# Performance work log

Measured on AMD Instinct MI355X. Metric: run time of the kernel, lower is better.

## Reference

```python
import jax, jax.numpy as jnp
import numpy as np
import math

B, S, H, NH, DH, FF, L = 2, 1024, 768, 12, 64, 3072, 4
LN_EPS = 1e-12


def _layer_norm(x, g, b):
    m = jnp.mean(x, axis=-1, keepdims=True)
    v = jnp.mean(jnp.square(x - m), axis=-1, keepdims=True)
    return (x - m) * jax.lax.rsqrt(v + LN_EPS) * g + b


def _gelu(x):
    # BERT erf-based gelu: x * 0.5 * (1 + erf(x / sqrt(2)))
    return x * 0.5 * (1.0 + jax.lax.erf(x / jnp.sqrt(jnp.asarray(2.0, x.dtype))))


def setup_inputs() -> dict:
    key = jax.random.key(0)
    ks = jax.random.split(key, 10)
    init = lambda k, shape: (jax.random.normal(k, shape, jnp.float32) * 0.02)
    inp = {
        'x': jax.random.normal(ks[0], (B, S, H), jnp.float32),
        'mask': jax.random.randint(ks[1], (B, S, S), 0, 2).astype(jnp.int32),
        'Wq': init(ks[2], (L, H, H)), 'bq': jnp.zeros((L, H), jnp.float32),
        'Wk': init(ks[3], (L, H, H)), 'bk': jnp.zeros((L, H), jnp.float32),
        'Wv': init(ks[4], (L, H, H)), 'bv': jnp.zeros((L, H), jnp.float32),
        'Wao': init(ks[5], (L, H, H)), 'bao': jnp.zeros((L, H), jnp.float32),
        'g1': jnp.ones((L, H), jnp.float32), 'b1': jnp.zeros((L, H), jnp.float32),
        'Wi': init(ks[6], (L, H, FF)), 'bi': jnp.zeros((L, FF), jnp.float32),
        'Wfo': init(ks[7], (L, FF, H)), 'bfo': jnp.zeros((L, H), jnp.float32),
        'g2': jnp.ones((L, H), jnp.float32), 'b2': jnp.zeros((L, H), jnp.float32),
    }
    return inp


def reference(x, mask, Wq, bq, Wk, bk, Wv, bv, Wao, bao, g1, b1, Wi, bi, Wfo, bfo, g2, b2):
    # additive mask: (1 - mask) * -10000, broadcast over heads -> [B,1,S,S]
    adder = (1.0 - mask.astype(x.dtype))[:, None, :, :] * -10000.0
    scale = 1.0 / math.sqrt(DH)

    def block(h, p):
        (wq, bq_, wk, bk_, wv, bv_, wao, bao_, g1_, b1_, wi, bi_, wfo, bfo_, g2_, b2_) = p
        q = (h @ wq + bq_).reshape(B, S, NH, DH)
        k = (h @ wk + bk_).reshape(B, S, NH, DH)
        v = (h @ wv + bv_).reshape(B, S, NH, DH)
        scores = jnp.einsum('bqhd,bkhd->bhqk', q, k) * scale + adder
        probs = jax.nn.softmax(scores, axis=-1)
        ctx = jnp.einsum('bhqk,bkhd->bqhd', probs, v).reshape(B, S, H)
        attn_out = _layer_norm(ctx @ wao + bao_ + h, g1_, b1_)
        inter = _gelu(attn_out @ wi + bi_)
        out = _layer_norm(inter @ wfo + bfo_ + attn_out, g2_, b2_)
        return out, None

    params = (Wq, bq, Wk, bk, Wv, bv, Wao, bao, g1, b1, Wi, bi, Wfo, bfo, g2, b2)
    out, _ = jax.lax.scan(block, x, params)
    return out
```

## Files before the change

kernel.cpp:

```cpp
#include <hip/hip_runtime.h>
#include <math.h>

#define B_  2
#define S_  1024
#define H_  768
#define NH_ 12
#define DH_ 64
#define FF_ 3072
#define L_  4

typedef short v8s __attribute__((ext_vector_type(8)));
typedef float v4f __attribute__((ext_vector_type(4)));

static __device__ __forceinline__ unsigned short f2bf(float f) {
    unsigned int u = __float_as_uint(f);
    unsigned int r = (u + 0x7fffu + ((u >> 16) & 1u)) >> 16;
    return (unsigned short)r;
}
static __device__ __forceinline__ float bf2f(unsigned short u) {
    return __uint_as_float((unsigned int)u << 16);
}

#define GLOAD16(g, l) __builtin_amdgcn_global_load_lds( \
    (const __attribute__((address_space(1))) unsigned int*)(g), \
    (__attribute__((address_space(3))) unsigned int*)(l), 16, 0, 0)

__global__ void conv_bf16_k(const float* __restrict__ in, unsigned short* __restrict__ out, int n) {
    int i = blockIdx.x * 256 + threadIdx.x;
    if (i < n) out[i] = f2bf(in[i]);
}

__global__ void maskconv_k(const int* __restrict__ m, unsigned short* __restrict__ o, int n) {
    int i = blockIdx.x * 256 + threadIdx.x;
    if (i < n) o[i] = m[i] ? (unsigned short)0u : (unsigned short)0xC661u;
}

__global__ __launch_bounds__(256) void transpose_convert(
    const float* __restrict__ W, unsigned short* __restrict__ Wt,
    int K, int N, size_t in_lstride, size_t out_lstride)
{
    __shared__ float tile[32][33];
    const int l = blockIdx.z;
    const float* src = W + (size_t)l * in_lstride;
    unsigned short* dst = Wt + (size_t)l * out_lstride;
    const int k0 = blockIdx.x * 32;
    const int n0 = blockIdx.y * 32;
    const int t = threadIdx.x;
    const int tc = t & 31, tr = t >> 5;
#pragma unroll
    for (int i = 0; i < 4; ++i) {
        int r = tr + i * 8;
        tile[r][tc] = src[(size_t)(k0 + r) * N + n0 + tc];
    }
    __syncthreads();
#pragma unroll
    for (int i = 0; i < 4; ++i) {
        int r = tr + i * 8;
        dst[(size_t)(n0 + r) * K + k0 + tc] = f2bf(tile[tc][r]);
    }
}

template<int ACT, int OUT_BF, int NBIAS, int SPLIT>
__global__ __launch_bounds__(256) void gemm_k(
    const unsigned short* __restrict__ A,
    const unsigned short* __restrict__ Bt,
    const float* __restrict__ b0,
    const float* __restrict__ b1,
    const float* __restrict__ b2,
    const float* __restrict__ res,
    void* __restrict__ out0,
    float* __restrict__ out1,
    int M, int N, int K, int klen)
{
    __shared__ __align__(16) unsigned short As[2][128 * 64];
    __shared__ __align__(16) unsigned short Bs[2][64 * 64];
    const int t = threadIdx.x;
    const int m0 = blockIdx.x * 128;
    const int n0 = blockIdx.y * 64;
    const int kz = SPLIT ? blockIdx.z : 0;
    const int kstart = kz * klen;
    const int lane = t & 63;
    const int w = t >> 6;
    const int wm = w >> 1, wn = w & 1;
    const int l15 = lane & 15;
    const int q4  = lane >> 4;

    const unsigned short* gA[4];
    const unsigned short* gB[2];
#pragma unroll
    for (int i = 0; i < 4; ++i) {
        int c = t + i * 256;
        int r = c >> 3, cc = c & 7;
        gA[i] = A + (size_t)(m0 + r) * K + kstart + ((cc ^ (r & 7)) << 3);
    }
#pragma unroll
    for (int i = 0; i < 2; ++i) {
        int c = t + i * 256;
        int r = c >> 3, cc = c & 7;
        gB[i] = Bt + (size_t)(n0 + r) * K + kstart + ((cc ^ (r & 7)) << 3);
    }
    const int ldsW = w * 512;

    v4f acc[4][2] = {};
    const int nt = klen >> 6;

#pragma unroll
    for (int i = 0; i < 4; ++i) GLOAD16(gA[i], &As[0][i * 2048 + ldsW]);
#pragma unroll
    for (int i = 0; i < 2; ++i) GLOAD16(gB[i], &Bs[0][i * 2048 + ldsW]);

    int cur = 0;
    for (int kt = 0; kt < nt; ++kt) {
        __syncthreads();
        if (kt + 1 < nt) {
            const size_t go = (size_t)(kt + 1) << 6;
#pragma unroll
            for (int i = 0; i < 4; ++i) GLOAD16(gA[i] + go, &As[cur ^ 1][i * 2048 + ldsW]);
#pragma unroll
            for (int i = 0; i < 2; ++i) GLOAD16(gB[i] + go, &Bs[cur ^ 1][i * 2048 + ldsW]);
        }
        const unsigned short* as = As[cur];
        const unsigned short* bs = Bs[cur];
#pragma unroll
        for (int ks = 0; ks < 2; ++ks) {
            v8s af[4], bf[2];
#pragma unroll
            for (int i = 0; i < 4; ++i) {
                int r = wm * 64 + i * 16 + l15;
                af[i] = *(const v8s*)&as[r * 64 + ((((ks << 2) + q4) ^ (r & 7)) << 3)];
            }
#pragma unroll
            for (int i = 0; i < 2; ++i) {
                int r = wn * 32 + i * 16 + l15;
                bf[i] = *(const v8s*)&bs[r * 64 + ((((ks << 2) + q4) ^ (r & 7)) << 3)];
            }
#pragma unroll
            for (int fm = 0; fm < 4; ++fm)
#pragma unroll
                for (int fn = 0; fn < 2; ++fn)
                    acc[fm][fn] = __builtin_amdgcn_mfma_f32_16x16x32_bf16(af[fm], bf[fn], acc[fm][fn], 0, 0, 0);
        }
        cur ^= 1;
    }

    const int rb = q4 * 4;
#pragma unroll
    for (int fm = 0; fm < 4; ++fm)
#pragma unroll
        for (int fn = 0; fn < 2; ++fn)
#pragma unroll
            for (int i = 0; i < 4; ++i) {
                const int row = m0 + wm * 64 + fm * 16 + rb + i;
                const int col = n0 + wn * 32 + fn * 16 + l15;
                float v = acc[fm][fn][i];
                const size_t oi = (size_t)row * N + col;
                if (!SPLIT || kz == 0) {
                    float bb;
                    if (NBIAS == 3) {
                        int which = (col >= 1536) ? 2 : (col >= 768 ? 1 : 0);
                        const float* bp = (which == 0) ? b0 : ((which == 1) ? b1 : b2);
                        bb = bp[col - which * 768];
                    } else {
                        bb = b0[col];
                    }
                    v += bb;
                    if (res) v += res[oi];
                    if (ACT == 1) v = 0.5f * v * (1.0f + erff(v * 0.70710678118654752f));
                    if (OUT_BF) ((unsigned short*)out0)[oi] = f2bf(v);
                    else        ((float*)out0)[oi] = v;
                } else {
                    out1[oi] = v;
                }
            }
}

__global__ __launch_bounds__(256) void ln_k(
    const float* __restrict__ ina, const float* __restrict__ inb,
    const float* __restrict__ g, const float* __restrict__ be,
    float* __restrict__ outf, unsigned short* __restrict__ outb)
{
    const int row = blockIdx.x;
    const float* xa = ina + (size_t)row * H_;
    const float* xb = inb + (size_t)row * H_;
    const int t = threadIdx.x;
    const int wave = t >> 6, lane = t & 63;
    float v0 = xa[t] + xb[t];
    float v1 = xa[t + 256] + xb[t + 256];
    float v2 = xa[t + 512] + xb[t + 512];
    float s = v0 + v1 + v2;
    float s2 = v0 * v0 + v1 * v1 + v2 * v2;
#pragma unroll
    for (int o = 32; o; o >>= 1) { s += __shfl_xor(s, o); s2 += __shfl_xor(s2, o); }
    __shared__ float rs[4], rq[4];
    if (lane == 0) { rs[wave] = s; rq[wave] = s2; }
    __syncthreads();
    s  = rs[0] + rs[1] + rs[2] + rs[3];
    s2 = rq[0] + rq[1] + rq[2] + rq[3];
    const float mean = s * (1.0f / 768.0f);
    float var = s2 * (1.0f / 768.0f) - mean * mean;
    var = fmaxf(var, 0.0f);
    const float inv = rsqrtf(var + 1e-12f);
#pragma unroll
    for (int i = 0; i < 3; ++i) {
        int c = t + i * 256;
        float vv = (i == 0) ? v0 : ((i == 1) ? v1 : v2);
        float y = (vv - mean) * inv * g[c] + be[c];
        outf[(size_t)row * H_ + c] = y;
        outb[(size_t)row * H_ + c] = f2bf(y);
    }
}

__global__ __launch_bounds__(256) void fattn_k(
    const unsigned short* __restrict__ qkv,
    const unsigned short* __restrict__ madd,
    float* __restrict__ pO,
    float* __restrict__ pML)
{
    const int qt = blockIdx.x, h = blockIdx.y, zz = blockIdx.z;
    const int b = zz >> 1, kvh = zz & 1;
    const int q0 = qt * 64;
    const int t = threadIdx.x;
    const int w = t >> 6, lane = t & 63;
    const int l15 = lane & 15;
    const int kr8 = (lane >> 4) * 8;
    const int rb  = (lane >> 4) * 4;
    const int wq0 = w * 16;

    __shared__ __align__(16) unsigned short Ks[64][72];
    __shared__ __align__(16) unsigned short Vt[4096];
    __shared__ __align__(16) unsigned short Ps[64][72];

    const size_t rstr = 2304;
    const unsigned short* base = qkv + (size_t)b * S_ * rstr + h * 64;

    v8s qf0, qf1;
    {
        const unsigned short* qp = base + (size_t)(q0 + wq0 + l15) * rstr + kr8;
        qf0 = *(const v8s*)qp;
        qf1 = *(const v8s*)(qp + 32);
    }

    const int skp = t >> 3;
    const int sd0 = (t & 7) * 8;
    const unsigned short* kbase = base + 768  + (size_t)(kvh * 512 + skp) * rstr + sd0;
    const unsigned short* vbase = base + 1536 + (size_t)(kvh * 512 + 2 * skp) * rstr + sd0;
    const size_t kstep = (size_t)64 * rstr;

    float m_[4], l_[4];
    v4f accO[4];
#pragma unroll
    for (int i = 0; i < 4; ++i) { m_[i] = -3.0e38f; l_[i] = 0.f; }
#pragma unroll
    for (int f = 0; f < 4; ++f) accO[f] = (v4f){0.f, 0.f, 0.f, 0.f};

    const unsigned short* mrow[4];
#pragma unroll
    for (int i = 0; i < 4; ++i)
        mrow[i] = madd + ((size_t)(b * S_) + q0 + wq0 + rb + i) * S_ + kvh * 512;

    v8s kA0, kA1, vA0, vA1, kB0, kB1, vB0, vB1;
    kA0 = *(const v8s*)(kbase);
    kA1 = *(const v8s*)(kbase + 32 * rstr);
    vA0 = *(const v8s*)(vbase);
    vA1 = *(const v8s*)(vbase + rstr);

    const float SC2 = 0.18033688011112042f;

    for (int kt = 0; kt < 8; ++kt) {
        const int k0 = kt * 64;
        unsigned short mu[16];
#pragma unroll
        for (int f = 0; f < 4; ++f)
#pragma unroll
            for (int i = 0; i < 4; ++i)
                mu[f * 4 + i] = mrow[i][k0 + f * 16 + l15];

        __syncthreads();
        if ((kt & 1) == 0) {
            *(v8s*)&Ks[skp][sd0] = kA0;
            *(v8s*)&Ks[skp + 32][sd0] = kA1;
#pragma unroll
            for (int j = 0; j < 8; ++j) {
                const int d = sd0 + j;
                const int sw = ((d & 7) ^ (d >> 3)) << 3;
                unsigned int pk = ((unsigned int)(unsigned short)vA1[j] << 16) | (unsigned short)vA0[j];
                *(unsigned int*)&Vt[(size_t)d * 64 + ((2 * skp) ^ sw)] = pk;
            }
            if (kt < 7) {
                const unsigned short* kp = kbase + (size_t)(kt + 1) * kstep;
                const unsigned short* vp = vbase + (size_t)(kt + 1) * kstep;
                kB0 = *(const v8s*)kp;
                kB1 = *(const v8s*)(kp + 32 * rstr);
                vB0 = *(const v8s*)vp;
                vB1 = *(const v8s*)(vp + rstr);
            }
        } else {
            *(v8s*)&Ks[skp][sd0] = kB0;
            *(v8s*)&Ks[skp + 32][sd0] = kB1;
#pragma unroll
            for (int j = 0; j < 8; ++j) {
                const int d = sd0 + j;
                const int sw = ((d & 7) ^ (d >> 3)) << 3;
                unsigned int pk = ((unsigned int)(unsigned short)vB1[j] << 16) | (unsigned short)vB0[j];
                *(unsigned int*)&Vt[(size_t)d * 64 + ((2 * skp) ^ sw)] = pk;
            }
            if (kt < 7) {
                const unsigned short* kp = kbase + (size_t)(kt + 1) * kstep;
                const unsigned short* vp = vbase + (size_t)(kt + 1) * kstep;
                kA0 = *(const v8s*)kp;
                kA1 = *(const v8s*)(kp + 32 * rstr);
                vA0 = *(const v8s*)vp;
                vA1 = *(const v8s*)(vp + rstr);
            }
        }
        __syncthreads();

        v4f s4[4];
#pragma unroll
        for (int f = 0; f < 4; ++f) s4[f] = (v4f){0.f, 0.f, 0.f, 0.f};
#pragma unroll
        for (int ks = 0; ks < 2; ++ks) {
            v8s qv = ks ? qf1 : qf0;
#pragma unroll
            for (int f = 0; f < 4; ++f) {
                v8s kf = *(const v8s*)&Ks[f * 16 + l15][ks * 32 + kr8];
                s4[f] = __builtin_amdgcn_mfma_f32_16x16x32_bf16(qv, kf, s4[f], 0, 0, 0);
            }
        }

        float p[4][4];
        float mx[4];
#pragma unroll
        for (int i = 0; i < 4; ++i) mx[i] = -3.0e38f;
#pragma unroll
        for (int f = 0; f < 4; ++f)
#pragma unroll
            for (int i = 0; i < 4; ++i) {
                float v = s4[f][i] * SC2 + bf2f(mu[f * 4 + i]);
                p[f][i] = v;
                mx[i] = fmaxf(mx[i], v);
            }
#pragma unroll
        for (int o = 8; o; o >>= 1)
#pragma unroll
            for (int i = 0; i < 4; ++i) mx[i] = fmaxf(mx[i], __shfl_xor(mx[i], o));
        float corr[4], rsum[4];
#pragma unroll
        for (int i = 0; i < 4; ++i) {
            float mn = fmaxf(m_[i], mx[i]);
            corr[i] = exp2f(m_[i] - mn);
            m_[i] = mn;
            rsum[i] = 0.f;
        }
#pragma unroll
        for (int f = 0; f < 4; ++f)
#pragma unroll
            for (int i = 0; i < 4; ++i) {
                float e = exp2f(p[f][i] - m_[i]);
                p[f][i] = e;
                rsum[i] += e;
            }
#pragma unroll
        for (int o = 8; o; o >>= 1)
#pragma unroll
            for (int i = 0; i < 4; ++i) rsum[i] += __shfl_xor(rsum[i], o);
#pragma unroll
        for (int i = 0; i < 4; ++i) l_[i] = l_[i] * corr[i] + rsum[i];
#pragma unroll
        for (int f = 0; f < 4; ++f)
#pragma unroll
            for (int i = 0; i < 4; ++i) accO[f][i] *= corr[i];

#pragma unroll
        for (int f = 0; f < 4; ++f)
#pragma unroll
            for (int i = 0; i < 4; ++i)
                Ps[wq0 + rb + i][f * 16 + l15] = f2bf(p[f][i]);

#pragma unroll
        for (int ks = 0; ks < 2; ++ks) {
            v8s pf = *(const v8s*)&Ps[wq0 + l15][ks * 32 + kr8];
#pragma unroll
            for (int f = 0; f < 4; ++f) {
                const int d = f * 16 + l15;
                const int sw = ((d & 7) ^ (d >> 3)) << 3;
                v8s vf = *(const v8s*)&Vt[(size_t)d * 64 + ((ks * 32 + kr8) ^ sw)];
                accO[f] = __builtin_amdgcn_mfma_f32_16x16x32_bf16(pf, vf, accO[f], 0, 0, 0);
            }
        }
    }

    float* po = pO + (size_t)kvh * (2048 * 768);
#pragma unroll
    for (int f = 0; f < 4; ++f)
#pragma unroll
        for (int i = 0; i < 4; ++i) {
            size_t row = (size_t)(b * S_) + q0 + wq0 + rb + i;
            po[row * 768 + h * 64 + f * 16 + l15] = accO[f][i];
        }
    if (l15 == 0) {
#pragma unroll
        for (int i = 0; i < 4; ++i) {
            size_t row = (size_t)(b * S_) + q0 + wq0 + rb + i;
            size_t idx = (((size_t)kvh * 2048 + row) * NH_ + h) * 2;
            pML[idx] = m_[i];
            pML[idx + 1] = l_[i];
        }
    }
}

__global__ __launch_bounds__(256) void attn_merge(
    const float* __restrict__ pO, const float* __restrict__ pML,
    unsigned short* __restrict__ ctx)
{
    const int i = blockIdx.x * 256 + threadIdx.x;
    const int row = i / 192;
    const int c4 = (i - row * 192) * 4;
    const int h = c4 >> 6;
    const size_t mi0 = ((size_t)row * NH_ + h) * 2;
    const size_t mi1 = (((size_t)2048 + row) * NH_ + h) * 2;
    const float m0 = pML[mi0], l0 = pML[mi0 + 1];
    const float m1 = pML[mi1], l1 = pML[mi1 + 1];
    const float mm = fmaxf(m0, m1);
    const float c0 = exp2f(m0 - mm), c1 = exp2f(m1 - mm);
    const float inv = 1.0f / (l0 * c0 + l1 * c1);
    const size_t off = (size_t)row * 768 + c4;
    float4 o0 = *(const float4*)&pO[off];
    float4 o1 = *(const float4*)&pO[(size_t)2048 * 768 + off];
    unsigned short r[4];
    r[0] = f2bf((o0.x * c0 + o1.x * c1) * inv);
    r[1] = f2bf((o0.y * c0 + o1.y * c1) * inv);
    r[2] = f2bf((o0.z * c0 + o1.z * c1) * inv);
    r[3] = f2bf((o0.w * c0 + o1.w * c1) * inv);
    *(uint2*)&ctx[off] = *(uint2*)r;
}

extern "C" void kernel_launch(void* const* d_in, const int* in_sizes, int n_in,
                              void* d_out, int out_size, void* d_ws, size_t ws_size,
                              hipStream_t stream)
{
    const float* x   = (const float*)d_in[0];
    const int*   mask= (const int*)  d_in[1];
    const float* Wq  = (const float*)d_in[2];
    const float* bq  = (const float*)d_in[3];
    const float* Wk  = (const float*)d_in[4];
    const float* bk  = (const float*)d_in[5];
    const float* Wv  = (const float*)d_in[6];
    const float* bv  = (const float*)d_in[7];
    const float* Wao = (const float*)d_in[8];
    const float* bao = (const float*)d_in[9];
    const float* g1  = (const float*)d_in[10];
    const float* b1  = (const float*)d_in[11];
    const float* Wi  = (const float*)d_in[12];
    const float* bi  = (const float*)d_in[13];
    const float* Wfo = (const float*)d_in[14];
    const float* bfo = (const float*)d_in[15];
    const float* g2  = (const float*)d_in[16];
    const float* b2  = (const float*)d_in[17];
    float* out = (float*)d_out;

    const int M = B_ * S_;
    char* basep = (char*)d_ws;
    size_t off = 0;
    auto alloc = [&](size_t bytes) -> char* {
        char* p = basep + off;
        off = (off + bytes + 255) & ~(size_t)255;
        return p;
    };

    unsigned short* WqkvT = (unsigned short*)alloc((size_t)L_ * 2304 * 768 * 2);
    unsigned short* WaoT  = (unsigned short*)alloc((size_t)L_ * 768 * 768 * 2);
    unsigned short* WiT   = (unsigned short*)alloc((size_t)L_ * 3072 * 768 * 2);
    unsigned short* WfoT  = (unsigned short*)alloc((size_t)L_ * 768 * 3072 * 2);
    unsigned short* h_bf  = (unsigned short*)alloc((size_t)M * 768 * 2);
    unsigned short* qkvbf = (unsigned short*)alloc((size_t)M * 2304 * 2);
    unsigned short* ctxbf = (unsigned short*)alloc((size_t)M * 768 * 2);
    float* t1a            = (float*)alloc((size_t)M * 768 * 4);
    float* attnf          = (float*)alloc((size_t)M * 768 * 4);
    unsigned short* attnbf= (unsigned short*)alloc((size_t)M * 768 * 2);
    unsigned short* interbf = (unsigned short*)alloc((size_t)M * FF_ * 2);
    unsigned short* madd  = (unsigned short*)alloc((size_t)B_ * S_ * S_ * 2);
    float* t1b = (float*)(void*)qkvbf;
    float* pO  = (float*)(void*)interbf;
    float* pML = t1a;

    dim3 tb(256);
    transpose_convert<<<dim3(24, 24, L_), tb, 0, stream>>>(Wq,  WqkvT + 0,          768,  768, (size_t)768 * 768,  (size_t)2304 * 768);
    transpose_convert<<<dim3(24, 24, L_), tb, 0, stream>>>(Wk,  WqkvT + 768 * 768,  768,  768, (size_t)768 * 768,  (size_t)2304 * 768);
    transpose_convert<<<dim3(24, 24, L_), tb, 0, stream>>>(Wv,  WqkvT + 1536 * 768, 768,  768, (size_t)768 * 768,  (size_t)2304 * 768);
    transpose_convert<<<dim3(24, 24, L_), tb, 0, stream>>>(Wao, WaoT,               768,  768, (size_t)768 * 768,  (size_t)768 * 768);
    transpose_convert<<<dim3(24, 96, L_), tb, 0, stream>>>(Wi,  WiT,                768, 3072, (size_t)768 * 3072, (size_t)3072 * 768);
    transpose_convert<<<dim3(96, 24, L_), tb, 0, stream>>>(Wfo, WfoT,              3072,  768, (size_t)3072 * 768, (size_t)768 * 3072);

    conv_bf16_k<<<(M * 768 + 255) / 256, 256, 0, stream>>>(x, h_bf, M * 768);
    maskconv_k<<<(B_ * S_ * S_ + 255) / 256, 256, 0, stream>>>(mask, madd, B_ * S_ * S_);

    const float* hres = x;
    for (int l = 0; l < L_; ++l) {
        gemm_k<0, 1, 3, 0><<<dim3(16, 36), tb, 0, stream>>>(
            h_bf, WqkvT + (size_t)l * 2304 * 768,
            bq + l * 768, bk + l * 768, bv + l * 768, nullptr, qkvbf, nullptr, M, 2304, 768, 768);
        fattn_k<<<dim3(S_ / 64, NH_, B_ * 2), tb, 0, stream>>>(qkvbf, madd, pO, pML);
        attn_merge<<<1536, tb, 0, stream>>>(pO, pML, ctxbf);
        gemm_k<0, 0, 1, 1><<<dim3(16, 12, 2), tb, 0, stream>>>(
            ctxbf, WaoT + (size_t)l * 768 * 768,
            bao + l * 768, nullptr, nullptr, hres, t1a, t1b, M, 768, 768, 384);
        ln_k<<<M, tb, 0, stream>>>(t1a, t1b, g1 + l * 768, b1 + l * 768, attnf, attnbf);
        gemm_k<1, 1, 1, 0><<<dim3(16, 48), tb, 0, stream>>>(
            attnbf, WiT + (size_t)l * 3072 * 768,
            bi + l * 3072, nullptr, nullptr, nullptr, interbf, nullptr, M, 3072, 768, 768);
        gemm_k<0, 0, 1, 1><<<dim3(16, 12, 2), tb, 0, stream>>>(
            interbf, WfoT + (size_t)l * 3072 * 768,
            bfo + l * 768, nullptr, nullptr, attnf, t1a, t1b, M, 768, 3072, 1536);
        ln_k<<<M, tb, 0, stream>>>(t1a, t1b, g2 + l * 768, b2 + l * 768, out, h_bf);
        hres = out;
    }
}
```

Measured before the change: 734.1 us.

## Deepen GEMM pipeline to 4-stage BK=32, remap workgroups across XCDs, lazy softmax rescale

The GEMM kernel drops from a double-buffered BK=64 loop to a 4-buffer BK=32 pipeline with compile-time K length, explicit vmcnt waits and raw barriers, so three tiles of global loads stay in flight. Workgroup IDs are remapped so consecutive tiles land on the same XCD, aiming for better L2 reuse. In flash attention, the running-max correction is applied only when some row max grows by more than a threshold, which skips exp and rescaling work on most iterations. The trade-offs are more LDS stages with smaller MFMA work per barrier, and a lazy-rescale scheme that depends on the threshold to keep values from overflowing.

```diff
diff --git a/kernel.cpp b/kernel.cpp
--- a/kernel.cpp
+++ b/kernel.cpp
@@ -60,7 +60,7 @@
     }
 }
 
-template<int ACT, int OUT_BF, int NBIAS, int SPLIT>
+template<int ACT, int OUT_BF, int NBIAS, int SPLIT, int KLEN>
 __global__ __launch_bounds__(256) void gemm_k(
     const unsigned short* __restrict__ A,
     const unsigned short* __restrict__ Bt,
@@ -70,78 +70,82 @@
     const float* __restrict__ res,
     void* __restrict__ out0,
     float* __restrict__ out1,
-    int M, int N, int K, int klen)
+    int M, int N, int K)
 {
-    __shared__ __align__(16) unsigned short As[2][128 * 64];
-    __shared__ __align__(16) unsigned short Bs[2][64 * 64];
+    constexpr int NT = KLEN / 32;
+    __shared__ __align__(16) unsigned short As[4][128 * 32];
+    __shared__ __align__(16) unsigned short Bs[4][64 * 32];
     const int t = threadIdx.x;
-    const int m0 = blockIdx.x * 128;
-    const int n0 = blockIdx.y * 64;
-    const int kz = SPLIT ? blockIdx.z : 0;
-    const int kstart = kz * klen;
+
+    const int nbx = gridDim.x, nby = gridDim.y;
+    int flat = ((int)blockIdx.z * nby + (int)blockIdx.y) * nbx + (int)blockIdx.x;
+    const int nwg = nbx * nby * (int)gridDim.z;
+    flat = (flat & 7) * (nwg >> 3) + (flat >> 3);
+    const int bx = flat % nbx;
+    const int rem = flat / nbx;
+    const int by = rem % nby;
+    const int kz = SPLIT ? (rem / nby) : 0;
+
+    const int m0 = bx * 128;
+    const int n0 = by * 64;
+    const int kstart = kz * KLEN;
     const int lane = t & 63;
     const int w = t >> 6;
     const int wm = w >> 1, wn = w & 1;
     const int l15 = lane & 15;
     const int q4  = lane >> 4;
 
-    const unsigned short* gA[4];
-    const unsigned short* gB[2];
-#pragma unroll
-    for (int i = 0; i < 4; ++i) {
-        int c = t + i * 256;
-        int r = c >> 3, cc = c & 7;
-        gA[i] = A + (size_t)(m0 + r) * K + kstart + ((cc ^ (r & 7)) << 3);
-    }
-#pragma unroll
-    for (int i = 0; i < 2; ++i) {
-        int c = t + i * 256;
-        int r = c >> 3, cc = c & 7;
-        gB[i] = Bt + (size_t)(n0 + r) * K + kstart + ((cc ^ (r & 7)) << 3);
-    }
-    const int ldsW = w * 512;
+    const int rA0 = t >> 2;
+    const int rA1 = 64 + (t >> 2);
+    const int csA0 = (((t & 3) ^ ((rA0 >> 1) & 3)) << 3);
+    const int csA1 = (((t & 3) ^ ((rA1 >> 1) & 3)) << 3);
+    const unsigned short* gA0 = A  + (size_t)(m0 + rA0) * K + kstart + csA0;
+    const unsigned short* gA1 = A  + (size_t)(m0 + rA1) * K + kstart + csA1;
+    const unsigned short* gB0 = Bt + (size_t)(n0 + rA0) * K + kstart + csA0;
+    const int aslot0 = t * 8, aslot1 = t * 8 + 2048, bslot = t * 8;
+
+#define STAGE_T(bi, kt_) do { \
+    const size_t go_ = (size_t)(kt_) * 32; \
+    GLOAD16(gA0 + go_, &As[bi][aslot0]); \
+    GLOAD16(gA1 + go_, &As[bi][aslot1]); \
+    GLOAD16(gB0 + go_, &Bs[bi][bslot]); \
+} while (0)
 
     v4f acc[4][2] = {};
-    const int nt = klen >> 6;
-
-#pragma unroll
-    for (int i = 0; i < 4; ++i) GLOAD16(gA[i], &As[0][i * 2048 + ldsW]);
-#pragma unroll
-    for (int i = 0; i < 2; ++i) GLOAD16(gB[i], &Bs[0][i * 2048 + ldsW]);
-
-    int cur = 0;
-    for (int kt = 0; kt < nt; ++kt) {
-        __syncthreads();
-        if (kt + 1 < nt) {
-            const size_t go = (size_t)(kt + 1) << 6;
-#pragma unroll
-            for (int i = 0; i < 4; ++i) GLOAD16(gA[i] + go, &As[cur ^ 1][i * 2048 + ldsW]);
-#pragma unroll
-            for (int i = 0; i < 2; ++i) GLOAD16(gB[i] + go, &Bs[cur ^ 1][i * 2048 + ldsW]);
-        }
-        const unsigned short* as = As[cur];
-        const unsigned short* bs = Bs[cur];
-#pragma unroll
-        for (int ks = 0; ks < 2; ++ks) {
-            v8s af[4], bf[2];
-#pragma unroll
-            for (int i = 0; i < 4; ++i) {
-                int r = wm * 64 + i * 16 + l15;
-                af[i] = *(const v8s*)&as[r * 64 + ((((ks << 2) + q4) ^ (r & 7)) << 3)];
-            }
-#pragma unroll
-            for (int i = 0; i < 2; ++i) {
-                int r = wn * 32 + i * 16 + l15;
-                bf[i] = *(const v8s*)&bs[r * 64 + ((((ks << 2) + q4) ^ (r & 7)) << 3)];
-            }
-#pragma unroll
-            for (int fm = 0; fm < 4; ++fm)
-#pragma unroll
-                for (int fn = 0; fn < 2; ++fn)
-                    acc[fm][fn] = __builtin_amdgcn_mfma_f32_16x16x32_bf16(af[fm], bf[fn], acc[fm][fn], 0, 0, 0);
-        }
-        cur ^= 1;
-    }
+    const int swz = (l15 >> 1) & 3;
+
+    STAGE_T(0, 0);
+    STAGE_T(1, 1);
+    STAGE_T(2, 2);
+
+#pragma unroll
+    for (int kt = 0; kt < NT; ++kt) {
+        if (kt < NT - 2)      asm volatile("s_waitcnt vmcnt(6)" ::: "memory");
+        else if (kt == NT - 2) asm volatile("s_waitcnt vmcnt(3)" ::: "memory");
+        else                   asm volatile("s_waitcnt vmcnt(0)" ::: "memory");
+        __builtin_amdgcn_s_barrier();
+        if (kt + 3 < NT) STAGE_T((kt + 3) & 3, kt + 3);
+
+        const unsigned short* as = As[kt & 3];
+        const unsigned short* bs = Bs[kt & 3];
+        v8s af[4], bf[2];
+#pragma unroll
+        for (int i = 0; i < 4; ++i) {
+            int r = wm * 64 + i * 16 + l15;
+            af[i] = *(const v8s*)&as[r * 32 + ((q4 ^ swz) << 3)];
+        }
+#pragma unroll
+        for (int i = 0; i < 2; ++i) {
+            int r = wn * 32 + i * 16 + l15;
+            bf[i] = *(const v8s*)&bs[r * 32 + ((q4 ^ swz) << 3)];
+        }
+#pragma unroll
+        for (int fm = 0; fm < 4; ++fm)
+#pragma unroll
+            for (int fn = 0; fn < 2; ++fn)
+                acc[fm][fn] = __builtin_amdgcn_mfma_f32_16x16x32_bf16(af[fm], bf[fn], acc[fm][fn], 0, 0, 0);
+    }
+#undef STAGE_T
 
     const int rb = q4 * 4;
 #pragma unroll
@@ -344,14 +348,21 @@
         for (int o = 8; o; o >>= 1)
 #pragma unroll
             for (int i = 0; i < 4; ++i) mx[i] = fmaxf(mx[i], __shfl_xor(mx[i], o));
-        float corr[4], rsum[4];
-#pragma unroll
-        for (int i = 0; i < 4; ++i) {
-            float mn = fmaxf(m_[i], mx[i]);
-            corr[i] = exp2f(m_[i] - mn);
-            m_[i] = mn;
-            rsum[i] = 0.f;
-        }
+        bool need = false;
+#pragma unroll
+        for (int i = 0; i < 4; ++i) need = need || (mx[i] > m_[i] + 8.0f);
+        if (__any((int)need)) {
+#pragma unroll
+            for (int i = 0; i < 4; ++i) {
+                float mn = fmaxf(m_[i], mx[i]);
+                float corr = exp2f(m_[i] - mn);
+                m_[i] = mn;
+                l_[i] *= corr;
+#pragma unroll
+                for (int f = 0; f < 4; ++f) accO[f][i] *= corr;
+            }
+        }
+        float rsum[4] = {0.f, 0.f, 0.f, 0.f};
 #pragma unroll
         for (int f = 0; f < 4; ++f)
 #pragma unroll
@@ -365,11 +376,7 @@
 #pragma unroll
             for (int i = 0; i < 4; ++i) rsum[i] += __shfl_xor(rsum[i], o);
 #pragma unroll
-        for (int i = 0; i < 4; ++i) l_[i] = l_[i] * corr[i] + rsum[i];
-#pragma unroll
-        for (int f = 0; f < 4; ++f)
-#pragma unroll
-            for (int i = 0; i < 4; ++i) accO[f][i] *= corr[i];
+        for (int i = 0; i < 4; ++i) l_[i] += rsum[i];
 
 #pragma unroll
         for (int f = 0; f < 4; ++f)
@@ -497,21 +504,21 @@
 
     const float* hres = x;
     for (int l = 0; l < L_; ++l) {
-        gemm_k<0, 1, 3, 0><<<dim3(16, 36), tb, 0, stream>>>(
+        gemm_k<0, 1, 3, 0, 768><<<dim3(16, 36), tb, 0, stream>>>(
             h_bf, WqkvT + (size_t)l * 2304 * 768,
-            bq + l * 768, bk + l * 768, bv + l * 768, nullptr, qkvbf, nullptr, M, 2304, 768, 768);
+            bq + l * 768, bk + l * 768, bv + l * 768, nullptr, qkvbf, nullptr, M, 2304, 768);
         fattn_k<<<dim3(S_ / 64, NH_, B_ * 2), tb, 0, stream>>>(qkvbf, madd, pO, pML);
         attn_merge<<<1536, tb, 0, stream>>>(pO, pML, ctxbf);
-        gemm_k<0, 0, 1, 1><<<dim3(16, 12, 2), tb, 0, stream>>>(
+        gemm_k<0, 0, 1, 1, 384><<<dim3(16, 12, 2), tb, 0, stream>>>(
             ctxbf, WaoT + (size_t)l * 768 * 768,
-            bao + l * 768, nullptr, nullptr, hres, t1a, t1b, M, 768, 768, 384);
+            bao + l * 768, nullptr, nullptr, hres, t1a, t1b, M, 768, 768);
         ln_k<<<M, tb, 0, stream>>>(t1a, t1b, g1 + l * 768, b1 + l * 768, attnf, attnbf);
-        gemm_k<1, 1, 1, 0><<<dim3(16, 48), tb, 0, stream>>>(
+        gemm_k<1, 1, 1, 0, 768><<<dim3(16, 48), tb, 0, stream>>>(
             attnbf, WiT + (size_t)l * 3072 * 768,
-            bi + l * 3072, nullptr, nullptr, nullptr, interbf, nullptr, M, 3072, 768, 768);
-        gemm_k<0, 0, 1, 1><<<dim3(16, 12, 2), tb, 0, stream>>>(
+            bi + l * 3072, nullptr, nullptr, nullptr, interbf, nullptr, M, 3072, 768);
+        gemm_k<0, 0, 1, 1, 1536><<<dim3(16, 12, 2), tb, 0, stream>>>(
             interbf, WfoT + (size_t)l * 3072 * 768,
-            bfo + l * 768, nullptr, nullptr, attnf, t1a, t1b, M, 768, 3072, 1536);
+            bfo + l * 768, nullptr, nullptr, attnf, t1a, t1b, M, 768, 3072);
         ln_k<<<M, tb, 0, stream>>>(t1a, t1b, g2 + l * 768, b2 + l * 768, out, h_bf);
         hres = out;
     }
```

Result: slower. 820.7 us (+11.8%).
